# Performance work log

Measured on AMD Instinct MI355X. Metric: run time of the kernel, lower is better.

The kernel has to match this reference:

```python
import jax, jax.numpy as jnp
import numpy as np

N = 1000      # num_nodes (<= max_nodes=1000 so the dense matrix path runs)
D = 128       # input_dim
H = 128       # hidden_dim
K = 10        # num_clusters
E = 500000    # num_edges
TEMP = 1.0
EPS = 1e-5    # torch LayerNorm default eps


def setup_inputs() -> dict:
    key = jax.random.key(0)
    ks = jax.random.split(key, 10)
    w = lambda k, shape: jax.random.normal(k, shape, jnp.float32) * 0.05
    return {
        "x": jax.random.normal(ks[0], (N, D), jnp.float32),
        "edge_index": jax.random.randint(ks[1], (2, E), 0, N, dtype=jnp.int32),
        # cluster_net: Linear(D,H) LN ReLU Linear(H,H//2) LN ReLU Linear(H//2,K)
        "w1": w(ks[2], (D, H)), "b1": jnp.zeros((H,), jnp.float32),
        "g1": jnp.ones((H,), jnp.float32), "be1": jnp.zeros((H,), jnp.float32),
        "w2": w(ks[3], (H, H // 2)), "b2": jnp.zeros((H // 2,), jnp.float32),
        "g2": jnp.ones((H // 2,), jnp.float32), "be2": jnp.zeros((H // 2,), jnp.float32),
        "w3": w(ks[4], (H // 2, K)), "b3": jnp.zeros((K,), jnp.float32),
        # complementarity_net: Linear(2D,H) LN ReLU Linear(H,1) Tanh
        "cw1": w(ks[5], (2 * D, H)), "cb1": jnp.zeros((H,), jnp.float32),
        "cg1": jnp.ones((H,), jnp.float32), "cbe1": jnp.zeros((H,), jnp.float32),
        "cw2": w(ks[6], (H, 1)), "cb2": jnp.zeros((1,), jnp.float32),
        "prototypes": jax.random.normal(ks[7], (K, D), jnp.float32),
    }


def _ln(x, g, b):
    m = x.mean(-1, keepdims=True)
    v = ((x - m) ** 2).mean(-1, keepdims=True)
    return (x - m) * jax.lax.rsqrt(v + EPS) * g + b


def _forward(x, w1, b1, g1, be1, w2, b2, g2, be2, w3, b3,
             cw1, cb1, cg1, cbe1, cw2, cb2, prototypes, edge_index):
    # --- cluster_net (dropout inactive in eval) ---
    h = jax.nn.relu(_ln(x @ w1 + b1, g1, be1))
    h = jax.nn.relu(_ln(h @ w2 + b2, g2, be2))
    cluster_logits = h @ w3 + b3                       # [N, K]
    cluster_probs = jax.nn.softmax(cluster_logits / TEMP, axis=-1)

    # --- complementarity scores on edges: gather + MLP ---
    row, col = edge_index[0], edge_index[1]
    ef = jnp.concatenate([x[row], x[col]], axis=-1)    # [E, 2D]
    he = jax.nn.relu(_ln(ef @ cw1 + cb1, cg1, cbe1))   # [E, H]
    comp_scores = jnp.tanh(he @ cw2 + cb2)[:, 0]       # [E]

    # --- cluster centers from soft assignments ---
    weighted_sum = cluster_probs.T @ x                 # [K, D]
    weights_sum = cluster_probs.sum(0)[:, None] + 1e-8
    cluster_centers = weighted_sum / weights_sum

    # --- dense all-pairs complementarity matrix (N <= 1000) ---
    # concat([x_i, x_j]) @ cw1 == x_i @ cw1[:D] + x_j @ cw1[D:]
    hi = x @ cw1[:D]                                   # [N, H]
    hj = x @ cw1[D:]                                   # [N, H]
    hp = hi[:, None, :] + hj[None, :, :] + cb1         # [N, N, H]
    hp = jax.nn.relu(_ln(hp, cg1, cbe1))
    comp_matrix = jnp.tanh(hp @ cw2 + cb2)[..., 0]     # [N, N]

    return cluster_logits, cluster_probs, comp_scores, comp_matrix, cluster_centers, prototypes


def reference(x, edge_index, w1, b1, g1, be1, w2, b2, g2, be2, w3, b3,
              cw1, cb1, cg1, cbe1, cw2, cb2, prototypes):
    return _forward(x, w1, b1, g1, be1, w2, b2, g2, be2, w3, b3,
                    cw1, cb1, cg1, cbe1, cw2, cb2, prototypes, edge_index)
```

## Files before the change

kernel.cpp:

```cpp
#include <hip/hip_runtime.h>
#include <hip/hip_bf16.h>
#include <math.h>

#define NN 1000
#define DD 128
#define HH 128
#define H2 64
#define KK 10
#define EE 500000
#define LN_EPS 1e-5f

typedef float v2f __attribute__((ext_vector_type(2)));

#define OFF_LOGITS  0
#define OFF_PROBS   10000
#define OFF_SCORES  20000
#define OFF_MATRIX  520000
#define OFF_CENTERS 1520000
#define OFF_PROTO   1521280

__device__ __forceinline__ unsigned int pack_bf16x2(float a, float b) {
  unsigned int ua = __float_as_uint(a);
  unsigned int ub = __float_as_uint(b);
  ua = (ua + 0x7FFFu + ((ua >> 16) & 1u)) >> 16;
  ub = (ub + 0x7FFFu + ((ub >> 16) & 1u)) & 0xFFFF0000u;
  return ua | ub;
}

__device__ __forceinline__ v2f unpk(unsigned int u) {
  v2f r;
  r.x = __uint_as_float(u << 16);
  r.y = __uint_as_float(u & 0xFFFF0000u);
  return r;
}

__global__ __launch_bounds__(256) void k1_split(
    const float* __restrict__ x,
    const float* __restrict__ w1, const float* __restrict__ b1,
    const float* __restrict__ g1, const float* __restrict__ be1,
    const float* __restrict__ w2, const float* __restrict__ b2,
    const float* __restrict__ g2, const float* __restrict__ be2,
    const float* __restrict__ w3, const float* __restrict__ b3,
    const float* __restrict__ cw1, const float* __restrict__ cb1,
    float* __restrict__ out_logits, float* __restrict__ out_probs,
    float* __restrict__ hi, float* __restrict__ hjbT,
    float* __restrict__ Srow, float* __restrict__ Qrow,
    float* __restrict__ Tcol, float* __restrict__ Rcol) {
  const int b = blockIdx.x;
  const int t = threadIdx.x;

  if (b < NN) {
    __shared__ float sx[DD];
    __shared__ float red[8];
    if (t < 32) *(float4*)&sx[4 * t] = *(const float4*)&x[b * DD + 4 * t];
    __syncthreads();

    float a0 = 0.f, a1 = 0.f, a2 = 0.f, a3 = 0.f;
    const float* wcol = (t < 128) ? (cw1 + t) : (cw1 + DD * HH + (t - 128));
#pragma unroll 8
    for (int d = 0; d < DD; d += 4) {
      const float4 xv = *(const float4*)&sx[d];
      a0 = fmaf(xv.x, wcol[(d + 0) * HH], a0);
      a1 = fmaf(xv.y, wcol[(d + 1) * HH], a1);
      a2 = fmaf(xv.z, wcol[(d + 2) * HH], a2);
      a3 = fmaf(xv.w, wcol[(d + 3) * HH], a3);
    }
    float acc = (a0 + a1) + (a2 + a3);
    if (t >= 128) acc += cb1[t - 128];
    if (t < 128) hi[b * HH + t] = acc;
    else         hjbT[(t - 128) * NN + b] = acc;

    float s = acc, q = acc * acc;
#pragma unroll
    for (int o = 1; o < 64; o <<= 1) {
      s += __shfl_xor(s, o, 64);
      q += __shfl_xor(q, o, 64);
    }
    const int wid = t >> 6;
    if ((t & 63) == 0) { red[wid * 2] = s; red[wid * 2 + 1] = q; }
    __syncthreads();
    if (t == 0)   { Srow[b] = red[0] + red[2]; Qrow[b] = red[1] + red[3]; }
    if (t == 128) { Tcol[b] = red[4] + red[6]; Rcol[b] = red[5] + red[7]; }
  } else {
    __shared__ float sx2[2][DD];
    __shared__ float shh[2][HH];
    __shared__ float sh2[2][H2];
    __shared__ float redc[8];
    __shared__ float slg2[2][16];
    const int m = b - NN;
    const int r0 = 2 * m;
    if (t < 32)      *(float4*)&sx2[0][4 * t] = *(const float4*)&x[r0 * DD + 4 * t];
    else if (t < 64) *(float4*)&sx2[1][4 * (t - 32)] =
                         *(const float4*)&x[(r0 + 1) * DD + 4 * (t - 32)];
    __syncthreads();

    const int row = t >> 7;
    const int col = t & 127;

    float a0 = 0.f, a1 = 0.f, a2 = 0.f, a3 = 0.f;
    const float* wc = w1 + col;
#pragma unroll 8
    for (int d = 0; d < DD; d += 4) {
      const float4 xv = *(const float4*)&sx2[row][d];
      a0 = fmaf(xv.x, wc[(d + 0) * HH], a0);
      a1 = fmaf(xv.y, wc[(d + 1) * HH], a1);
      a2 = fmaf(xv.z, wc[(d + 2) * HH], a2);
      a3 = fmaf(xv.w, wc[(d + 3) * HH], a3);
    }
    float acc = (a0 + a1) + (a2 + a3) + b1[col];
    {
      float s = acc, q = acc * acc;
#pragma unroll
      for (int o = 1; o < 64; o <<= 1) {
        s += __shfl_xor(s, o, 64);
        q += __shfl_xor(q, o, 64);
      }
      const int wid = t >> 6;
      if ((t & 63) == 0) { redc[wid * 2] = s; redc[wid * 2 + 1] = q; }
    }
    __syncthreads();
    {
      const float s = redc[4 * row] + redc[4 * row + 2];
      const float q = redc[4 * row + 1] + redc[4 * row + 3];
      const float mn = s * (1.0f / HH);
      const float var = q * (1.0f / HH) - mn * mn;
      const float rs = rsqrtf(var + LN_EPS);
      shh[row][col] = fmaxf(fmaf((acc - mn) * rs, g1[col], be1[col]), 0.0f);
    }
    __syncthreads();

    if (t < 128) {
      const int rw = t >> 6, c2 = t & 63;
      float b0 = 0.f, b1_ = 0.f, b2_ = 0.f, b3_ = 0.f;
      const float* w2c = w2 + c2;
#pragma unroll 8
      for (int d = 0; d < HH; d += 4) {
        const float4 hv = *(const float4*)&shh[rw][d];
        b0 = fmaf(hv.x, w2c[(d + 0) * H2], b0);
        b1_ = fmaf(hv.y, w2c[(d + 1) * H2], b1_);
        b2_ = fmaf(hv.z, w2c[(d + 2) * H2], b2_);
        b3_ = fmaf(hv.w, w2c[(d + 3) * H2], b3_);
      }
      float av = (b0 + b1_) + (b2_ + b3_) + b2[c2];
      float s2 = av, q2 = av * av;
#pragma unroll
      for (int o = 1; o < 64; o <<= 1) {
        s2 += __shfl_xor(s2, o, 64);
        q2 += __shfl_xor(q2, o, 64);
      }
      const float m2 = s2 * (1.0f / H2);
      const float var2 = q2 * (1.0f / H2) - m2 * m2;
      const float rs2 = rsqrtf(var2 + LN_EPS);
      sh2[rw][c2] = fmaxf(fmaf((av - m2) * rs2, g2[c2], be2[c2]), 0.0f);
    }
    __syncthreads();

    if (t < 32) {
      const int rw = t >> 4, k = t & 15;
      if (k < KK) {
        float a3_ = b3[k];
#pragma unroll
        for (int d = 0; d < H2; ++d) a3_ = fmaf(sh2[rw][d], w3[d * KK + k], a3_);
        out_logits[(r0 + rw) * KK + k] = a3_;
        slg2[rw][k] = a3_;
      }
    }
    __syncthreads();
    if (t < 32) {
      const int rw = t >> 4, k = t & 15;
      if (k < KK) {
        float mx = -1e30f;
#pragma unroll
        for (int i = 0; i < KK; ++i) mx = fmaxf(mx, slg2[rw][i]);
        float den = 0.0f;
#pragma unroll
        for (int i = 0; i < KK; ++i) den += expf(slg2[rw][i] - mx);
        out_probs[(r0 + rw) * KK + k] = expf(slg2[rw][k] - mx) / den;
      }
    }
  }
}

#define NCB 8
#define NPB 125

__global__ __launch_bounds__(128) void k_centers_part(
    const float* __restrict__ x, const float* __restrict__ probs,
    float* __restrict__ pc, float* __restrict__ pw) {
  __shared__ float sp[NCB * KK];
  const int b = blockIdx.x;
  const int t = threadIdx.x;
  const int n0 = b * NCB;
  if (t < NCB * KK) sp[t] = probs[n0 * KK + t];
  __syncthreads();
  float acc[KK];
#pragma unroll
  for (int k = 0; k < KK; ++k) acc[k] = 0.0f;
#pragma unroll
  for (int nn = 0; nn < NCB; ++nn) {
    const float xv = x[(n0 + nn) * DD + t];
#pragma unroll
    for (int k = 0; k < KK; ++k) acc[k] = fmaf(sp[nn * KK + k], xv, acc[k]);
  }
#pragma unroll
  for (int k = 0; k < KK; ++k) pc[b * (KK * DD) + k * DD + t] = acc[k];
  if (t < KK) {
    float s = 0.0f;
#pragma unroll
    for (int nn = 0; nn < NCB; ++nn) s += sp[nn * KK + t];
    pw[b * 16 + t] = s;
  }
}

#define TI 64
#define TJ 32
#define LSTRA 130
#define BSTR 130

__global__ __launch_bounds__(256) void k_matrix(
    const float* __restrict__ hi, const float* __restrict__ hjbT,
    const float* __restrict__ Srow, const float* __restrict__ Qrow,
    const float* __restrict__ Tcol, const float* __restrict__ Rcol,
    const float* __restrict__ cg1, const float* __restrict__ cbe1,
    const float* __restrict__ cw2, const float* __restrict__ cb2,
    float* __restrict__ out_mat) {
  __shared__ float sa[TI * LSTRA];
  __shared__ unsigned int sbt[16 * BSTR];
  __shared__ float sg[HH], sbe[HH], sw[HH];
  const int t = threadIdx.x;
  const int j0 = blockIdx.x * TJ;
  const int i0 = blockIdx.y * TI;

  if (t < HH) { sg[t] = cg1[t]; sbe[t] = cbe1[t]; sw[t] = cw2[t]; }
#pragma unroll
  for (int it = 0; it < TI * HH / 256; ++it) {
    const int idx = it * 256 + t;
    const int r = idx >> 7, h = idx & 127;
    int gi = i0 + r; if (gi >= NN) gi = NN - 1;
    sa[r * LSTRA + h] = hi[gi * HH + h];
  }
  {
    const int cp = t & 15;
    const int hw = t >> 4;
    const int jc = j0 + 2 * cp;
    const int c0 = (jc < NN) ? jc : NN - 1;
    const int c1 = (jc + 1 < NN) ? jc + 1 : NN - 1;
#pragma unroll
    for (int hb = 0; hb < 8; ++hb) {
      const int h = hb * 16 + hw;
      sbt[cp * BSTR + h] = pack_bf16x2(hjbT[h * NN + c0], hjbT[h * NN + c1]);
    }
  }
  __syncthreads();

  const int tr = t >> 4, tc = t & 15;
  const int ia = 4 * tr;
  const int gi0 = i0 + ia;
  const int gj0 = j0 + 2 * tc;

  float Sr[4], Qr[4];
#pragma unroll
  for (int r = 0; r < 4; ++r) {
    const int gi = (gi0 + r < NN) ? gi0 + r : NN - 1;
    Sr[r] = Srow[gi]; Qr[r] = Qrow[gi];
  }
  const int c0 = (gj0 < NN) ? gj0 : NN - 1;
  const int c1 = (gj0 + 1 < NN) ? gj0 + 1 : NN - 1;
  const v2f Tc2 = (v2f){Tcol[c0], Tcol[c1]};
  const v2f Rc2 = (v2f){Rcol[c0], Rcol[c1]};

  v2f dt[4];
#pragma unroll
  for (int r = 0; r < 4; ++r) dt[r] = (v2f){0.f, 0.f};
#pragma unroll 4
  for (int h = 0; h < HH; h += 2) {
    const uint2 bb = *(const uint2*)&sbt[tc * BSTR + h];
    const v2f bx = unpk(bb.x), by = unpk(bb.y);
#pragma unroll
    for (int r = 0; r < 4; ++r) {
      const v2f av = *(const v2f*)&sa[(ia + r) * LSTRA + h];
      dt[r] += (v2f){av.x, av.x} * bx + (v2f){av.y, av.y} * by;
    }
  }

  const float inv = 1.0f / HH;
  v2f rrv[4], nmv[4];
#pragma unroll
  for (int r = 0; r < 4; ++r) {
    const v2f mu = (Sr[r] + Tc2) * inv;
    const v2f ev2 = (Qr[r] + Rc2 + 2.0f * dt[r]) * inv;
    const v2f var = ev2 - mu * mu;
    v2f rs;
    rs.x = rsqrtf(var.x + LN_EPS);
    rs.y = rsqrtf(var.y + LN_EPS);
    rrv[r] = rs;
    nmv[r] = -mu * rs;
  }

  v2f cc[4];
#pragma unroll
  for (int r = 0; r < 4; ++r) cc[r] = (v2f){0.f, 0.f};
  const v2f vzero = (v2f){0.f, 0.f};
#pragma unroll 4
  for (int h = 0; h < HH; h += 2) {
    const uint2 bb = *(const uint2*)&sbt[tc * BSTR + h];
    const v2f bx = unpk(bb.x), by = unpk(bb.y);
    const v2f gv = *(const v2f*)&sg[h];
    const v2f bev = *(const v2f*)&sbe[h];
    const v2f wv = *(const v2f*)&sw[h];
#pragma unroll
    for (int r = 0; r < 4; ++r) {
      const v2f av = *(const v2f*)&sa[(ia + r) * LSTRA + h];
      v2f v = (v2f){av.x, av.x} + bx;
      v2f z = v * rrv[r] + nmv[r];
      z = z * (v2f){gv.x, gv.x} + (v2f){bev.x, bev.x};
      z = __builtin_elementwise_max(z, vzero);
      cc[r] += z * (v2f){wv.x, wv.x};
      v = (v2f){av.y, av.y} + by;
      z = v * rrv[r] + nmv[r];
      z = z * (v2f){gv.y, gv.y} + (v2f){bev.y, bev.y};
      z = __builtin_elementwise_max(z, vzero);
      cc[r] += z * (v2f){wv.y, wv.y};
    }
  }

  const float cb = cb2[0];
  if (gj0 < NN) {
#pragma unroll
    for (int r = 0; r < 4; ++r) {
      const int gi = gi0 + r;
      if (gi < NN) {
        float2 o;
        o.x = tanhf(cc[r].x + cb);
        o.y = tanhf(cc[r].y + cb);
        *(float2*)&out_mat[gi * NN + gj0] = o;
      }
    }
  }
}

__global__ __launch_bounds__(256) void k_tail(
    const float* __restrict__ pc, const float* __restrict__ pw,
    const float* __restrict__ proto, const int* __restrict__ ei,
    const float* __restrict__ mat,
    float* __restrict__ out_centers, float* __restrict__ out_proto,
    float* __restrict__ out_scores) {
  const int b = blockIdx.x;
  const int t = threadIdx.x;
  if (b < KK) {
    __shared__ float sred[128];
    const int k = b;
    if (t < 128) sred[t] = (t < NPB) ? pw[t * 16 + k] : 0.0f;
    __syncthreads();
    for (int o = 64; o > 0; o >>= 1) {
      if (t < o) sred[t] += sred[t + o];
      __syncthreads();
    }
    if (t < 128) {
      const float wsum = sred[0] + 1e-8f;
      float acc = 0.0f;
#pragma unroll 5
      for (int bb = 0; bb < NPB; ++bb) acc += pc[bb * (KK * DD) + k * DD + t];
      out_centers[k * DD + t] = acc / wsum;
      out_proto[k * DD + t] = proto[k * DD + t];
    }
  } else {
    const int e = (b - KK) * 256 + t;
    if (e < EE) {
      const int r = ei[e];
      const int c = ei[EE + e];
      out_scores[e] = mat[r * NN + c];
    }
  }
}

extern "C" void kernel_launch(void* const* d_in, const int* in_sizes, int n_in,
                              void* d_out, int out_size, void* d_ws, size_t ws_size,
                              hipStream_t stream) {
  const float* x    = (const float*)d_in[0];
  const int*   ei   = (const int*)d_in[1];
  const float* w1   = (const float*)d_in[2];
  const float* b1   = (const float*)d_in[3];
  const float* g1   = (const float*)d_in[4];
  const float* be1  = (const float*)d_in[5];
  const float* w2   = (const float*)d_in[6];
  const float* b2   = (const float*)d_in[7];
  const float* g2   = (const float*)d_in[8];
  const float* be2  = (const float*)d_in[9];
  const float* w3   = (const float*)d_in[10];
  const float* b3   = (const float*)d_in[11];
  const float* cw1  = (const float*)d_in[12];
  const float* cb1  = (const float*)d_in[13];
  const float* cg1  = (const float*)d_in[14];
  const float* cbe1 = (const float*)d_in[15];
  const float* cw2  = (const float*)d_in[16];
  const float* cb2  = (const float*)d_in[17];
  const float* prot = (const float*)d_in[18];

  float* out        = (float*)d_out;
  float* out_logits = out + OFF_LOGITS;
  float* out_probs  = out + OFF_PROBS;
  float* out_scores = out + OFF_SCORES;
  float* out_mat    = out + OFF_MATRIX;
  float* out_cent   = out + OFF_CENTERS;
  float* out_proto  = out + OFF_PROTO;

  float* hi   = (float*)d_ws;
  float* hjbT = hi + NN * HH;
  float* Srow = hjbT + NN * HH;
  float* Qrow = Srow + NN;
  float* Tcol = Qrow + NN;
  float* Rcol = Tcol + NN;
  float* pc   = Rcol + NN;
  float* pw   = pc + NPB * KK * DD;

  k1_split<<<NN + NN / 2, 256, 0, stream>>>(
      x, w1, b1, g1, be1, w2, b2, g2, be2, w3, b3, cw1, cb1,
      out_logits, out_probs, hi, hjbT, Srow, Qrow, Tcol, Rcol);
  k_centers_part<<<NPB, 128, 0, stream>>>(x, out_probs, pc, pw);
  dim3 g3((NN + TJ - 1) / TJ, (NN + TI - 1) / TI);
  k_matrix<<<g3, 256, 0, stream>>>(hi, hjbT, Srow, Qrow, Tcol, Rcol,
                                   cg1, cbe1, cw2, cb2, out_mat);
  k_tail<<<KK + (EE + 255) / 256, 256, 0, stream>>>(pc, pw, prot, ei, out_mat,
                                                    out_cent, out_proto, out_scores);
}
```

Before: 62.79 us.

## Store hi as bf16 and enlarge matrix tile to 64x64 with 4x4 microtile

The first kernel now writes the per-node hi projection packed as bf16 pairs, halving that buffer and its load traffic. The matrix kernel grows its j-tile from 32 to 64 columns, so each thread computes 4 rows by 4 columns. The B tile is stored h-major and the A tile as packed bf16, which gives more reuse per shared-memory load in both the dot-product and LayerNorm/ReLU passes. The LayerNorm gamma, beta and output weights are now read straight from global memory instead of shared memory. Rounding hi to bf16 adds precision error, and the larger tile launches half as many blocks and uses more registers per thread.

```diff
diff --git a/kernel.cpp b/kernel.cpp
--- a/kernel.cpp
+++ b/kernel.cpp
@@ -11,6 +11,7 @@
 #define LN_EPS 1e-5f
 
 typedef float v2f __attribute__((ext_vector_type(2)));
+typedef unsigned int uint;
 
 #define OFF_LOGITS  0
 #define OFF_PROBS   10000
@@ -19,15 +20,15 @@
 #define OFF_CENTERS 1520000
 #define OFF_PROTO   1521280
 
-__device__ __forceinline__ unsigned int pack_bf16x2(float a, float b) {
-  unsigned int ua = __float_as_uint(a);
-  unsigned int ub = __float_as_uint(b);
+__device__ __forceinline__ uint pack_bf16x2(float a, float b) {
+  uint ua = __float_as_uint(a);
+  uint ub = __float_as_uint(b);
   ua = (ua + 0x7FFFu + ((ua >> 16) & 1u)) >> 16;
   ub = (ub + 0x7FFFu + ((ub >> 16) & 1u)) & 0xFFFF0000u;
   return ua | ub;
 }
 
-__device__ __forceinline__ v2f unpk(unsigned int u) {
+__device__ __forceinline__ v2f unpk(uint u) {
   v2f r;
   r.x = __uint_as_float(u << 16);
   r.y = __uint_as_float(u & 0xFFFF0000u);
@@ -43,7 +44,7 @@
     const float* __restrict__ w3, const float* __restrict__ b3,
     const float* __restrict__ cw1, const float* __restrict__ cb1,
     float* __restrict__ out_logits, float* __restrict__ out_probs,
-    float* __restrict__ hi, float* __restrict__ hjbT,
+    uint* __restrict__ hi_bf, float* __restrict__ hjbT,
     float* __restrict__ Srow, float* __restrict__ Qrow,
     float* __restrict__ Tcol, float* __restrict__ Rcol) {
   const int b = blockIdx.x;
@@ -67,8 +68,12 @@
     }
     float acc = (a0 + a1) + (a2 + a3);
     if (t >= 128) acc += cb1[t - 128];
-    if (t < 128) hi[b * HH + t] = acc;
-    else         hjbT[(t - 128) * NN + b] = acc;
+    if (t < 128) {
+      const float other = __shfl_xor(acc, 1, 64);
+      if ((t & 1) == 0) hi_bf[b * 64 + (t >> 1)] = pack_bf16x2(acc, other);
+    } else {
+      hjbT[(t - 128) * NN + b] = acc;
+    }
 
     float s = acc, q = acc * acc;
 #pragma unroll
@@ -213,42 +218,40 @@
 }
 
 #define TI 64
-#define TJ 32
-#define LSTRA 130
-#define BSTR 130
+#define TJ 64
+#define SA_STR 66
+#define SB_STR 34
 
 __global__ __launch_bounds__(256) void k_matrix(
-    const float* __restrict__ hi, const float* __restrict__ hjbT,
+    const uint* __restrict__ hi_bf, const float* __restrict__ hjbT,
     const float* __restrict__ Srow, const float* __restrict__ Qrow,
     const float* __restrict__ Tcol, const float* __restrict__ Rcol,
     const float* __restrict__ cg1, const float* __restrict__ cbe1,
     const float* __restrict__ cw2, const float* __restrict__ cb2,
     float* __restrict__ out_mat) {
-  __shared__ float sa[TI * LSTRA];
-  __shared__ unsigned int sbt[16 * BSTR];
-  __shared__ float sg[HH], sbe[HH], sw[HH];
+  __shared__ uint sa[TI * SA_STR];
+  __shared__ uint sbt[HH * SB_STR];
   const int t = threadIdx.x;
   const int j0 = blockIdx.x * TJ;
   const int i0 = blockIdx.y * TI;
 
-  if (t < HH) { sg[t] = cg1[t]; sbe[t] = cbe1[t]; sw[t] = cw2[t]; }
-#pragma unroll
-  for (int it = 0; it < TI * HH / 256; ++it) {
+#pragma unroll
+  for (int it = 0; it < 8; ++it) {
     const int idx = it * 256 + t;
-    const int r = idx >> 7, h = idx & 127;
+    const int r = idx >> 5, w2 = idx & 31;
     int gi = i0 + r; if (gi >= NN) gi = NN - 1;
-    sa[r * LSTRA + h] = hi[gi * HH + h];
+    *(uint2*)&sa[r * SA_STR + 2 * w2] = *(const uint2*)&hi_bf[gi * 64 + 2 * w2];
   }
   {
-    const int cp = t & 15;
-    const int hw = t >> 4;
+    const int cp = t & 31;
+    const int hw = t >> 5;
     const int jc = j0 + 2 * cp;
     const int c0 = (jc < NN) ? jc : NN - 1;
     const int c1 = (jc + 1 < NN) ? jc + 1 : NN - 1;
 #pragma unroll
-    for (int hb = 0; hb < 8; ++hb) {
-      const int h = hb * 16 + hw;
-      sbt[cp * BSTR + h] = pack_bf16x2(hjbT[h * NN + c0], hjbT[h * NN + c1]);
+    for (int hb = 0; hb < 16; ++hb) {
+      const int h = hb * 8 + hw;
+      sbt[h * SB_STR + cp] = pack_bf16x2(hjbT[h * NN + c0], hjbT[h * NN + c1]);
     }
   }
   __syncthreads();
@@ -256,7 +259,7 @@
   const int tr = t >> 4, tc = t & 15;
   const int ia = 4 * tr;
   const int gi0 = i0 + ia;
-  const int gj0 = j0 + 2 * tc;
+  const int gj0 = j0 + 4 * tc;
 
   float Sr[4], Qr[4];
 #pragma unroll
@@ -264,63 +267,93 @@
     const int gi = (gi0 + r < NN) ? gi0 + r : NN - 1;
     Sr[r] = Srow[gi]; Qr[r] = Qrow[gi];
   }
-  const int c0 = (gj0 < NN) ? gj0 : NN - 1;
-  const int c1 = (gj0 + 1 < NN) ? gj0 + 1 : NN - 1;
-  const v2f Tc2 = (v2f){Tcol[c0], Tcol[c1]};
-  const v2f Rc2 = (v2f){Rcol[c0], Rcol[c1]};
-
-  v2f dt[4];
-#pragma unroll
-  for (int r = 0; r < 4; ++r) dt[r] = (v2f){0.f, 0.f};
-#pragma unroll 4
-  for (int h = 0; h < HH; h += 2) {
-    const uint2 bb = *(const uint2*)&sbt[tc * BSTR + h];
-    const v2f bx = unpk(bb.x), by = unpk(bb.y);
+  v2f Tc2[2], Rc2[2];
+#pragma unroll
+  for (int p = 0; p < 2; ++p) {
+    const int ca = (gj0 + 2 * p < NN) ? gj0 + 2 * p : NN - 1;
+    const int cbx = (gj0 + 2 * p + 1 < NN) ? gj0 + 2 * p + 1 : NN - 1;
+    Tc2[p] = (v2f){Tcol[ca], Tcol[cbx]};
+    Rc2[p] = (v2f){Rcol[ca], Rcol[cbx]};
+  }
+
+  v2f dt[4][2];
+#pragma unroll
+  for (int r = 0; r < 4; ++r) { dt[r][0] = (v2f){0, 0}; dt[r][1] = (v2f){0, 0}; }
+
+#pragma unroll 2
+  for (int h = 0; h < HH; h += 4) {
+    float ar[4][4];
 #pragma unroll
     for (int r = 0; r < 4; ++r) {
-      const v2f av = *(const v2f*)&sa[(ia + r) * LSTRA + h];
-      dt[r] += (v2f){av.x, av.x} * bx + (v2f){av.y, av.y} * by;
+      const uint2 au = *(const uint2*)&sa[(ia + r) * SA_STR + (h >> 1)];
+      const v2f a01 = unpk(au.x), a23 = unpk(au.y);
+      ar[r][0] = a01.x; ar[r][1] = a01.y; ar[r][2] = a23.x; ar[r][3] = a23.y;
+    }
+#pragma unroll
+    for (int hh = 0; hh < 4; ++hh) {
+      const uint2 bu = *(const uint2*)&sbt[(h + hh) * SB_STR + 2 * tc];
+      const v2f b0 = unpk(bu.x), b1 = unpk(bu.y);
+#pragma unroll
+      for (int r = 0; r < 4; ++r) {
+        const v2f as = (v2f){ar[r][hh], ar[r][hh]};
+        dt[r][0] += as * b0;
+        dt[r][1] += as * b1;
+      }
     }
   }
 
   const float inv = 1.0f / HH;
-  v2f rrv[4], nmv[4];
-#pragma unroll
-  for (int r = 0; r < 4; ++r) {
-    const v2f mu = (Sr[r] + Tc2) * inv;
-    const v2f ev2 = (Qr[r] + Rc2 + 2.0f * dt[r]) * inv;
-    const v2f var = ev2 - mu * mu;
-    v2f rs;
-    rs.x = rsqrtf(var.x + LN_EPS);
-    rs.y = rsqrtf(var.y + LN_EPS);
-    rrv[r] = rs;
-    nmv[r] = -mu * rs;
-  }
-
-  v2f cc[4];
-#pragma unroll
-  for (int r = 0; r < 4; ++r) cc[r] = (v2f){0.f, 0.f};
+  v2f rrv[4][2], nmv[4][2];
+#pragma unroll
+  for (int r = 0; r < 4; ++r)
+#pragma unroll
+    for (int p = 0; p < 2; ++p) {
+      const v2f mu = (Sr[r] + Tc2[p]) * inv;
+      const v2f ev2 = (Qr[r] + Rc2[p] + 2.0f * dt[r][p]) * inv;
+      const v2f var = ev2 - mu * mu;
+      v2f rs;
+      rs.x = rsqrtf(var.x + LN_EPS);
+      rs.y = rsqrtf(var.y + LN_EPS);
+      rrv[r][p] = rs;
+      nmv[r][p] = -mu * rs;
+    }
+
+  v2f cc[4][2];
+#pragma unroll
+  for (int r = 0; r < 4; ++r) { cc[r][0] = (v2f){0, 0}; cc[r][1] = (v2f){0, 0}; }
   const v2f vzero = (v2f){0.f, 0.f};
-#pragma unroll 4
-  for (int h = 0; h < HH; h += 2) {
-    const uint2 bb = *(const uint2*)&sbt[tc * BSTR + h];
-    const v2f bx = unpk(bb.x), by = unpk(bb.y);
-    const v2f gv = *(const v2f*)&sg[h];
-    const v2f bev = *(const v2f*)&sbe[h];
-    const v2f wv = *(const v2f*)&sw[h];
+
+#pragma unroll 2
+  for (int h = 0; h < HH; h += 4) {
+    float ar[4][4];
 #pragma unroll
     for (int r = 0; r < 4; ++r) {
-      const v2f av = *(const v2f*)&sa[(ia + r) * LSTRA + h];
-      v2f v = (v2f){av.x, av.x} + bx;
-      v2f z = v * rrv[r] + nmv[r];
-      z = z * (v2f){gv.x, gv.x} + (v2f){bev.x, bev.x};
-      z = __builtin_elementwise_max(z, vzero);
-      cc[r] += z * (v2f){wv.x, wv.x};
-      v = (v2f){av.y, av.y} + by;
-      z = v * rrv[r] + nmv[r];
-      z = z * (v2f){gv.y, gv.y} + (v2f){bev.y, bev.y};
-      z = __builtin_elementwise_max(z, vzero);
-      cc[r] += z * (v2f){wv.y, wv.y};
+      const uint2 au = *(const uint2*)&sa[(ia + r) * SA_STR + (h >> 1)];
+      const v2f a01 = unpk(au.x), a23 = unpk(au.y);
+      ar[r][0] = a01.x; ar[r][1] = a01.y; ar[r][2] = a23.x; ar[r][3] = a23.y;
+    }
+#pragma unroll
+    for (int hh = 0; hh < 4; ++hh) {
+      const uint2 bu = *(const uint2*)&sbt[(h + hh) * SB_STR + 2 * tc];
+      const v2f b0 = unpk(bu.x), b1 = unpk(bu.y);
+      const float g_ = cg1[h + hh];
+      const float be_ = cbe1[h + hh];
+      const float w_ = cw2[h + hh];
+      const v2f gs = (v2f){g_, g_};
+      const v2f bes = (v2f){be_, be_};
+      const v2f wss = (v2f){w_, w_};
+#pragma unroll
+      for (int r = 0; r < 4; ++r) {
+        const v2f as = (v2f){ar[r][hh], ar[r][hh]};
+        v2f z0 = (as + b0) * rrv[r][0] + nmv[r][0];
+        z0 = z0 * gs + bes;
+        z0 = __builtin_elementwise_max(z0, vzero);
+        cc[r][0] += z0 * wss;
+        v2f z1 = (as + b1) * rrv[r][1] + nmv[r][1];
+        z1 = z1 * gs + bes;
+        z1 = __builtin_elementwise_max(z1, vzero);
+        cc[r][1] += z1 * wss;
+      }
     }
   }
 
@@ -330,10 +363,12 @@
     for (int r = 0; r < 4; ++r) {
       const int gi = gi0 + r;
       if (gi < NN) {
-        float2 o;
-        o.x = tanhf(cc[r].x + cb);
-        o.y = tanhf(cc[r].y + cb);
-        *(float2*)&out_mat[gi * NN + gj0] = o;
+        float4 o;
+        o.x = tanhf(cc[r][0].x + cb);
+        o.y = tanhf(cc[r][0].y + cb);
+        o.z = tanhf(cc[r][1].x + cb);
+        o.w = tanhf(cc[r][1].y + cb);
+        *(float4*)&out_mat[gi * NN + gj0] = o;
       }
     }
   }
@@ -405,21 +440,21 @@
   float* out_cent   = out + OFF_CENTERS;
   float* out_proto  = out + OFF_PROTO;
 
-  float* hi   = (float*)d_ws;
-  float* hjbT = hi + NN * HH;
-  float* Srow = hjbT + NN * HH;
-  float* Qrow = Srow + NN;
-  float* Tcol = Qrow + NN;
-  float* Rcol = Tcol + NN;
-  float* pc   = Rcol + NN;
-  float* pw   = pc + NPB * KK * DD;
+  uint*  hi_bf = (uint*)d_ws;
+  float* hjbT  = (float*)d_ws + NN * 64;
+  float* Srow  = hjbT + NN * HH;
+  float* Qrow  = Srow + NN;
+  float* Tcol  = Qrow + NN;
+  float* Rcol  = Tcol + NN;
+  float* pc    = Rcol + NN;
+  float* pw    = pc + NPB * KK * DD;
 
   k1_split<<<NN + NN / 2, 256, 0, stream>>>(
       x, w1, b1, g1, be1, w2, b2, g2, be2, w3, b3, cw1, cb1,
-      out_logits, out_probs, hi, hjbT, Srow, Qrow, Tcol, Rcol);
+      out_logits, out_probs, hi_bf, hjbT, Srow, Qrow, Tcol, Rcol);
   k_centers_part<<<NPB, 128, 0, stream>>>(x, out_probs, pc, pw);
   dim3 g3((NN + TJ - 1) / TJ, (NN + TI - 1) / TI);
-  k_matrix<<<g3, 256, 0, stream>>>(hi, hjbT, Srow, Qrow, Tcol, Rcol,
+  k_matrix<<<g3, 256, 0, stream>>>(hi_bf, hjbT, Srow, Qrow, Tcol, Rcol,
                                    cg1, cbe1, cw2, cb2, out_mat);
   k_tail<<<KK + (EE + 255) / 256, 256, 0, stream>>>(pc, pw, prot, ei, out_mat,
                                                     out_cent, out_proto, out_scores);
```

New measurement: 67.10 us. 6.9% more time.

## Retile pairwise matrix kernel to 32x64 with fp32 column operand in LDS

Applied to the files above, without the earlier changes.

The pairwise complementarity kernel switches from a 64x32 tile with bf16-packed column features to a 32x64 tile that stores the column features as fp32 in LDS with an h-major layout. Each thread now computes 2 rows by 4 columns, reading float4 column vectors and writing float4 outputs. LN gamma, beta and weight now come from global/scalar loads instead of LDS. This drops the bf16 pack/unpack overhead and the precision loss, at the cost of a larger LDS footprint (about 51KB), which may reduce occupancy.

```diff
diff --git a/kernel.cpp b/kernel.cpp
--- a/kernel.cpp
+++ b/kernel.cpp
@@ -18,21 +18,6 @@
 #define OFF_MATRIX  520000
 #define OFF_CENTERS 1520000
 #define OFF_PROTO   1521280
-
-__device__ __forceinline__ unsigned int pack_bf16x2(float a, float b) {
-  unsigned int ua = __float_as_uint(a);
-  unsigned int ub = __float_as_uint(b);
-  ua = (ua + 0x7FFFu + ((ua >> 16) & 1u)) >> 16;
-  ub = (ub + 0x7FFFu + ((ub >> 16) & 1u)) & 0xFFFF0000u;
-  return ua | ub;
-}
-
-__device__ __forceinline__ v2f unpk(unsigned int u) {
-  v2f r;
-  r.x = __uint_as_float(u << 16);
-  r.y = __uint_as_float(u & 0xFFFF0000u);
-  return r;
-}
 
 __global__ __launch_bounds__(256) void k1_split(
     const float* __restrict__ x,
@@ -212,10 +197,10 @@
   }
 }
 
-#define TI 64
-#define TJ 32
-#define LSTRA 130
-#define BSTR 130
+#define TI 32
+#define TJ 64
+#define SA_STR 130
+#define SB_STR 68
 
 __global__ __launch_bounds__(256) void k_matrix(
     const float* __restrict__ hi, const float* __restrict__ hjbT,
@@ -224,116 +209,135 @@
     const float* __restrict__ cg1, const float* __restrict__ cbe1,
     const float* __restrict__ cw2, const float* __restrict__ cb2,
     float* __restrict__ out_mat) {
-  __shared__ float sa[TI * LSTRA];
-  __shared__ unsigned int sbt[16 * BSTR];
-  __shared__ float sg[HH], sbe[HH], sw[HH];
+  __shared__ float sa[TI * SA_STR];
+  __shared__ float sb[HH * SB_STR];
   const int t = threadIdx.x;
   const int j0 = blockIdx.x * TJ;
   const int i0 = blockIdx.y * TI;
 
-  if (t < HH) { sg[t] = cg1[t]; sbe[t] = cbe1[t]; sw[t] = cw2[t]; }
-#pragma unroll
-  for (int it = 0; it < TI * HH / 256; ++it) {
+#pragma unroll
+  for (int it = 0; it < 4; ++it) {
     const int idx = it * 256 + t;
-    const int r = idx >> 7, h = idx & 127;
+    const int r = idx >> 5, w = idx & 31;
     int gi = i0 + r; if (gi >= NN) gi = NN - 1;
-    sa[r * LSTRA + h] = hi[gi * HH + h];
+    *(float4*)&sa[r * SA_STR + 4 * w] = *(const float4*)&hi[gi * HH + 4 * w];
   }
   {
-    const int cp = t & 15;
-    const int hw = t >> 4;
-    const int jc = j0 + 2 * cp;
-    const int c0 = (jc < NN) ? jc : NN - 1;
-    const int c1 = (jc + 1 < NN) ? jc + 1 : NN - 1;
-#pragma unroll
-    for (int hb = 0; hb < 8; ++hb) {
-      const int h = hb * 16 + hw;
-      sbt[cp * BSTR + h] = pack_bf16x2(hjbT[h * NN + c0], hjbT[h * NN + c1]);
+    const int c = t & 63;
+    const int hw = t >> 6;
+    int gj = j0 + c; if (gj >= NN) gj = NN - 1;
+#pragma unroll
+    for (int hb = 0; hb < 32; ++hb) {
+      const int h = hb * 4 + hw;
+      sb[h * SB_STR + c] = hjbT[h * NN + gj];
     }
   }
   __syncthreads();
 
   const int tr = t >> 4, tc = t & 15;
-  const int ia = 4 * tr;
+  const int ia = 2 * tr;
+  const int ja = 4 * tc;
   const int gi0 = i0 + ia;
-  const int gj0 = j0 + 2 * tc;
-
-  float Sr[4], Qr[4];
-#pragma unroll
-  for (int r = 0; r < 4; ++r) {
+  const int gj0 = j0 + ja;
+
+  float Sr[2], Qr[2];
+#pragma unroll
+  for (int r = 0; r < 2; ++r) {
     const int gi = (gi0 + r < NN) ? gi0 + r : NN - 1;
     Sr[r] = Srow[gi]; Qr[r] = Qrow[gi];
   }
-  const int c0 = (gj0 < NN) ? gj0 : NN - 1;
-  const int c1 = (gj0 + 1 < NN) ? gj0 + 1 : NN - 1;
-  const v2f Tc2 = (v2f){Tcol[c0], Tcol[c1]};
-  const v2f Rc2 = (v2f){Rcol[c0], Rcol[c1]};
-
-  v2f dt[4];
-#pragma unroll
-  for (int r = 0; r < 4; ++r) dt[r] = (v2f){0.f, 0.f};
+  v2f Tc2[2], Rc2[2];
+#pragma unroll
+  for (int p = 0; p < 2; ++p) {
+    const int ca = (gj0 + 2 * p < NN) ? gj0 + 2 * p : NN - 1;
+    const int cb_ = (gj0 + 2 * p + 1 < NN) ? gj0 + 2 * p + 1 : NN - 1;
+    Tc2[p] = (v2f){Tcol[ca], Tcol[cb_]};
+    Rc2[p] = (v2f){Rcol[ca], Rcol[cb_]};
+  }
+
+  v2f dt[2][2];
+#pragma unroll
+  for (int r = 0; r < 2; ++r) { dt[r][0] = (v2f){0, 0}; dt[r][1] = (v2f){0, 0}; }
+
 #pragma unroll 4
   for (int h = 0; h < HH; h += 2) {
-    const uint2 bb = *(const uint2*)&sbt[tc * BSTR + h];
-    const v2f bx = unpk(bb.x), by = unpk(bb.y);
-#pragma unroll
-    for (int r = 0; r < 4; ++r) {
-      const v2f av = *(const v2f*)&sa[(ia + r) * LSTRA + h];
-      dt[r] += (v2f){av.x, av.x} * bx + (v2f){av.y, av.y} * by;
-    }
+    const v2f a0 = *(const v2f*)&sa[(ia + 0) * SA_STR + h];
+    const v2f a1 = *(const v2f*)&sa[(ia + 1) * SA_STR + h];
+    const float4 blo = *(const float4*)&sb[h * SB_STR + ja];
+    const float4 bhi = *(const float4*)&sb[(h + 1) * SB_STR + ja];
+    const v2f b0l = (v2f){blo.x, blo.y}, b1l = (v2f){blo.z, blo.w};
+    const v2f b0h = (v2f){bhi.x, bhi.y}, b1h = (v2f){bhi.z, bhi.w};
+    dt[0][0] += (v2f){a0.x, a0.x} * b0l + (v2f){a0.y, a0.y} * b0h;
+    dt[0][1] += (v2f){a0.x, a0.x} * b1l + (v2f){a0.y, a0.y} * b1h;
+    dt[1][0] += (v2f){a1.x, a1.x} * b0l + (v2f){a1.y, a1.y} * b0h;
+    dt[1][1] += (v2f){a1.x, a1.x} * b1l + (v2f){a1.y, a1.y} * b1h;
   }
 
   const float inv = 1.0f / HH;
-  v2f rrv[4], nmv[4];
-#pragma unroll
-  for (int r = 0; r < 4; ++r) {
-    const v2f mu = (Sr[r] + Tc2) * inv;
-    const v2f ev2 = (Qr[r] + Rc2 + 2.0f * dt[r]) * inv;
-    const v2f var = ev2 - mu * mu;
-    v2f rs;
-    rs.x = rsqrtf(var.x + LN_EPS);
-    rs.y = rsqrtf(var.y + LN_EPS);
-    rrv[r] = rs;
-    nmv[r] = -mu * rs;
-  }
-
-  v2f cc[4];
-#pragma unroll
-  for (int r = 0; r < 4; ++r) cc[r] = (v2f){0.f, 0.f};
+  v2f rrv[2][2], nmv[2][2];
+#pragma unroll
+  for (int r = 0; r < 2; ++r)
+#pragma unroll
+    for (int p = 0; p < 2; ++p) {
+      const v2f mu = (Sr[r] + Tc2[p]) * inv;
+      const v2f ev2 = (Qr[r] + Rc2[p] + 2.0f * dt[r][p]) * inv;
+      const v2f var = ev2 - mu * mu;
+      v2f rs;
+      rs.x = rsqrtf(var.x + LN_EPS);
+      rs.y = rsqrtf(var.y + LN_EPS);
+      rrv[r][p] = rs;
+      nmv[r][p] = -mu * rs;
+    }
+
+  v2f cc[2][2];
+#pragma unroll
+  for (int r = 0; r < 2; ++r) { cc[r][0] = (v2f){0, 0}; cc[r][1] = (v2f){0, 0}; }
   const v2f vzero = (v2f){0.f, 0.f};
+
 #pragma unroll 4
   for (int h = 0; h < HH; h += 2) {
-    const uint2 bb = *(const uint2*)&sbt[tc * BSTR + h];
-    const v2f bx = unpk(bb.x), by = unpk(bb.y);
-    const v2f gv = *(const v2f*)&sg[h];
-    const v2f bev = *(const v2f*)&sbe[h];
-    const v2f wv = *(const v2f*)&sw[h];
-#pragma unroll
-    for (int r = 0; r < 4; ++r) {
-      const v2f av = *(const v2f*)&sa[(ia + r) * LSTRA + h];
-      v2f v = (v2f){av.x, av.x} + bx;
-      v2f z = v * rrv[r] + nmv[r];
-      z = z * (v2f){gv.x, gv.x} + (v2f){bev.x, bev.x};
-      z = __builtin_elementwise_max(z, vzero);
-      cc[r] += z * (v2f){wv.x, wv.x};
-      v = (v2f){av.y, av.y} + by;
-      z = v * rrv[r] + nmv[r];
-      z = z * (v2f){gv.y, gv.y} + (v2f){bev.y, bev.y};
-      z = __builtin_elementwise_max(z, vzero);
-      cc[r] += z * (v2f){wv.y, wv.y};
+    const v2f a0 = *(const v2f*)&sa[(ia + 0) * SA_STR + h];
+    const v2f a1 = *(const v2f*)&sa[(ia + 1) * SA_STR + h];
+    const float4 blo = *(const float4*)&sb[h * SB_STR + ja];
+    const float4 bhi = *(const float4*)&sb[(h + 1) * SB_STR + ja];
+    const float g0 = cg1[h], g1_ = cg1[h + 1];
+    const float e0 = cbe1[h], e1 = cbe1[h + 1];
+    const float w0 = cw2[h], w1_ = cw2[h + 1];
+    const v2f b0l = (v2f){blo.x, blo.y}, b1l = (v2f){blo.z, blo.w};
+    const v2f b0h = (v2f){bhi.x, bhi.y}, b1h = (v2f){bhi.z, bhi.w};
+#pragma unroll
+    for (int r = 0; r < 2; ++r) {
+      const v2f ar = (r == 0) ? a0 : a1;
+      const v2f axl = (v2f){ar.x, ar.x};
+      const v2f axh = (v2f){ar.y, ar.y};
+#pragma unroll
+      for (int p = 0; p < 2; ++p) {
+        const v2f bl = (p == 0) ? b0l : b1l;
+        const v2f bh = (p == 0) ? b0h : b1h;
+        v2f z = (axl + bl) * rrv[r][p] + nmv[r][p];
+        z = z * (v2f){g0, g0} + (v2f){e0, e0};
+        z = __builtin_elementwise_max(z, vzero);
+        cc[r][p] += z * (v2f){w0, w0};
+        z = (axh + bh) * rrv[r][p] + nmv[r][p];
+        z = z * (v2f){g1_, g1_} + (v2f){e1, e1};
+        z = __builtin_elementwise_max(z, vzero);
+        cc[r][p] += z * (v2f){w1_, w1_};
+      }
     }
   }
 
   const float cb = cb2[0];
   if (gj0 < NN) {
 #pragma unroll
-    for (int r = 0; r < 4; ++r) {
+    for (int r = 0; r < 2; ++r) {
       const int gi = gi0 + r;
       if (gi < NN) {
-        float2 o;
-        o.x = tanhf(cc[r].x + cb);
-        o.y = tanhf(cc[r].y + cb);
-        *(float2*)&out_mat[gi * NN + gj0] = o;
+        float4 o;
+        o.x = tanhf(cc[r][0].x + cb);
+        o.y = tanhf(cc[r][0].y + cb);
+        o.z = tanhf(cc[r][1].x + cb);
+        o.w = tanhf(cc[r][1].y + cb);
+        *(float4*)&out_mat[gi * NN + gj0] = o;
       }
     }
   }
```

New measurement: 60.65 us. 3.4% less time.

## Store hi tile as bf16 in LDS, batch two rows per projection block

Applied to the files above, without the earlier changes.

The matrix kernel now packs the row-side hidden projections into bf16 pairs in shared memory, halving LDS footprint and traffic. Its inner loops read 128-bit chunks and process four hidden units per iteration. The LayerNorm gamma/beta and output weights are read straight from global memory instead of being staged in LDS. The projection kernel computes two nodes per block, so it reuses each loaded weight twice and launches half as many blocks. These changes trade the precision of hi (now bf16) for less LDS bandwidth and occupancy pressure.

```diff
diff --git a/kernel.cpp b/kernel.cpp
--- a/kernel.cpp
+++ b/kernel.cpp
@@ -11,6 +11,7 @@
 #define LN_EPS 1e-5f
 
 typedef float v2f __attribute__((ext_vector_type(2)));
+typedef unsigned int uint;
 
 #define OFF_LOGITS  0
 #define OFF_PROBS   10000
@@ -19,15 +20,15 @@
 #define OFF_CENTERS 1520000
 #define OFF_PROTO   1521280
 
-__device__ __forceinline__ unsigned int pack_bf16x2(float a, float b) {
-  unsigned int ua = __float_as_uint(a);
-  unsigned int ub = __float_as_uint(b);
+__device__ __forceinline__ uint pack_bf16x2(float a, float b) {
+  uint ua = __float_as_uint(a);
+  uint ub = __float_as_uint(b);
   ua = (ua + 0x7FFFu + ((ua >> 16) & 1u)) >> 16;
   ub = (ub + 0x7FFFu + ((ub >> 16) & 1u)) & 0xFFFF0000u;
   return ua | ub;
 }
 
-__device__ __forceinline__ v2f unpk(unsigned int u) {
+__device__ __forceinline__ v2f unpk(uint u) {
   v2f r;
   r.x = __uint_as_float(u << 16);
   r.y = __uint_as_float(u & 0xFFFF0000u);
@@ -49,45 +50,63 @@
   const int b = blockIdx.x;
   const int t = threadIdx.x;
 
-  if (b < NN) {
-    __shared__ float sx[DD];
-    __shared__ float red[8];
-    if (t < 32) *(float4*)&sx[4 * t] = *(const float4*)&x[b * DD + 4 * t];
-    __syncthreads();
-
-    float a0 = 0.f, a1 = 0.f, a2 = 0.f, a3 = 0.f;
-    const float* wcol = (t < 128) ? (cw1 + t) : (cw1 + DD * HH + (t - 128));
+  if (b < NN / 2) {
+    __shared__ float sx2[2][DD];
+    __shared__ float red[16];
+    const int r0 = 2 * b;
+    if (t < 64) {
+      const int rr = t >> 5, c4 = t & 31;
+      *(float4*)&sx2[rr][4 * c4] = *(const float4*)&x[(r0 + rr) * DD + 4 * c4];
+    }
+    __syncthreads();
+
+    const int col = t & 127;
+    const float* wcol = (t < 128) ? (cw1 + col) : (cw1 + DD * HH + col);
+    float p00 = 0.f, p01 = 0.f, p10 = 0.f, p11 = 0.f;
 #pragma unroll 8
-    for (int d = 0; d < DD; d += 4) {
-      const float4 xv = *(const float4*)&sx[d];
-      a0 = fmaf(xv.x, wcol[(d + 0) * HH], a0);
-      a1 = fmaf(xv.y, wcol[(d + 1) * HH], a1);
-      a2 = fmaf(xv.z, wcol[(d + 2) * HH], a2);
-      a3 = fmaf(xv.w, wcol[(d + 3) * HH], a3);
-    }
-    float acc = (a0 + a1) + (a2 + a3);
-    if (t >= 128) acc += cb1[t - 128];
-    if (t < 128) hi[b * HH + t] = acc;
-    else         hjbT[(t - 128) * NN + b] = acc;
-
-    float s = acc, q = acc * acc;
+    for (int d = 0; d < DD; d += 2) {
+      const float w0 = wcol[d * HH];
+      const float w1_ = wcol[(d + 1) * HH];
+      const float2 x0 = *(const float2*)&sx2[0][d];
+      const float2 x1 = *(const float2*)&sx2[1][d];
+      p00 = fmaf(x0.x, w0, p00); p01 = fmaf(x0.y, w1_, p01);
+      p10 = fmaf(x1.x, w0, p10); p11 = fmaf(x1.y, w1_, p11);
+    }
+    float acc0 = p00 + p01, acc1 = p10 + p11;
+    if (t >= 128) { const float cb_ = cb1[col]; acc0 += cb_; acc1 += cb_; }
+    if (t < 128) {
+      hi[(r0 + 0) * HH + col] = acc0;
+      hi[(r0 + 1) * HH + col] = acc1;
+    } else {
+      *(float2*)&hjbT[col * NN + r0] = (float2){acc0, acc1};
+    }
+    float s0 = acc0, q0 = acc0 * acc0, s1 = acc1, q1 = acc1 * acc1;
 #pragma unroll
     for (int o = 1; o < 64; o <<= 1) {
-      s += __shfl_xor(s, o, 64);
-      q += __shfl_xor(q, o, 64);
+      s0 += __shfl_xor(s0, o, 64); q0 += __shfl_xor(q0, o, 64);
+      s1 += __shfl_xor(s1, o, 64); q1 += __shfl_xor(q1, o, 64);
     }
     const int wid = t >> 6;
-    if ((t & 63) == 0) { red[wid * 2] = s; red[wid * 2 + 1] = q; }
-    __syncthreads();
-    if (t == 0)   { Srow[b] = red[0] + red[2]; Qrow[b] = red[1] + red[3]; }
-    if (t == 128) { Tcol[b] = red[4] + red[6]; Rcol[b] = red[5] + red[7]; }
+    if ((t & 63) == 0) {
+      red[wid * 4 + 0] = s0; red[wid * 4 + 1] = q0;
+      red[wid * 4 + 2] = s1; red[wid * 4 + 3] = q1;
+    }
+    __syncthreads();
+    if (t == 0) {
+      Srow[r0] = red[0] + red[4];  Qrow[r0] = red[1] + red[5];
+      Srow[r0 + 1] = red[2] + red[6]; Qrow[r0 + 1] = red[3] + red[7];
+    }
+    if (t == 128) {
+      Tcol[r0] = red[8] + red[12];  Rcol[r0] = red[9] + red[13];
+      Tcol[r0 + 1] = red[10] + red[14]; Rcol[r0 + 1] = red[11] + red[15];
+    }
   } else {
     __shared__ float sx2[2][DD];
     __shared__ float shh[2][HH];
     __shared__ float sh2[2][H2];
     __shared__ float redc[8];
     __shared__ float slg2[2][16];
-    const int m = b - NN;
+    const int m = b - NN / 2;
     const int r0 = 2 * m;
     if (t < 32)      *(float4*)&sx2[0][4 * t] = *(const float4*)&x[r0 * DD + 4 * t];
     else if (t < 64) *(float4*)&sx2[1][4 * (t - 32)] =
@@ -214,8 +233,8 @@
 
 #define TI 64
 #define TJ 32
-#define LSTRA 130
-#define BSTR 130
+#define SA_STR 66
+#define SB_STR 132
 
 __global__ __launch_bounds__(256) void k_matrix(
     const float* __restrict__ hi, const float* __restrict__ hjbT,
@@ -224,20 +243,19 @@
     const float* __restrict__ cg1, const float* __restrict__ cbe1,
     const float* __restrict__ cw2, const float* __restrict__ cb2,
     float* __restrict__ out_mat) {
-  __shared__ float sa[TI * LSTRA];
-  __shared__ unsigned int sbt[16 * BSTR];
-  __shared__ float sg[HH], sbe[HH], sw[HH];
+  __shared__ uint sa[TI * SA_STR];
+  __shared__ uint sb[16 * SB_STR];
   const int t = threadIdx.x;
   const int j0 = blockIdx.x * TJ;
   const int i0 = blockIdx.y * TI;
 
-  if (t < HH) { sg[t] = cg1[t]; sbe[t] = cbe1[t]; sw[t] = cw2[t]; }
-#pragma unroll
-  for (int it = 0; it < TI * HH / 256; ++it) {
+#pragma unroll
+  for (int it = 0; it < 16; ++it) {
     const int idx = it * 256 + t;
-    const int r = idx >> 7, h = idx & 127;
+    const int r = idx >> 6, w = idx & 63;
     int gi = i0 + r; if (gi >= NN) gi = NN - 1;
-    sa[r * LSTRA + h] = hi[gi * HH + h];
+    const float2 av = *(const float2*)&hi[gi * HH + 2 * w];
+    sa[r * SA_STR + w] = pack_bf16x2(av.x, av.y);
   }
   {
     const int cp = t & 15;
@@ -248,7 +266,7 @@
 #pragma unroll
     for (int hb = 0; hb < 8; ++hb) {
       const int h = hb * 16 + hw;
-      sbt[cp * BSTR + h] = pack_bf16x2(hjbT[h * NN + c0], hjbT[h * NN + c1]);
+      sb[cp * SB_STR + h] = pack_bf16x2(hjbT[h * NN + c0], hjbT[h * NN + c1]);
     }
   }
   __syncthreads();
@@ -264,22 +282,25 @@
     const int gi = (gi0 + r < NN) ? gi0 + r : NN - 1;
     Sr[r] = Srow[gi]; Qr[r] = Qrow[gi];
   }
-  const int c0 = (gj0 < NN) ? gj0 : NN - 1;
-  const int c1 = (gj0 + 1 < NN) ? gj0 + 1 : NN - 1;
-  const v2f Tc2 = (v2f){Tcol[c0], Tcol[c1]};
-  const v2f Rc2 = (v2f){Rcol[c0], Rcol[c1]};
+  const int cc0 = (gj0 < NN) ? gj0 : NN - 1;
+  const int cc1 = (gj0 + 1 < NN) ? gj0 + 1 : NN - 1;
+  const v2f Tc2 = (v2f){Tcol[cc0], Tcol[cc1]};
+  const v2f Rc2 = (v2f){Rcol[cc0], Rcol[cc1]};
 
   v2f dt[4];
 #pragma unroll
   for (int r = 0; r < 4; ++r) dt[r] = (v2f){0.f, 0.f};
-#pragma unroll 4
-  for (int h = 0; h < HH; h += 2) {
-    const uint2 bb = *(const uint2*)&sbt[tc * BSTR + h];
-    const v2f bx = unpk(bb.x), by = unpk(bb.y);
+
+#pragma unroll 2
+  for (int h = 0; h < HH; h += 4) {
+    const uint4 bu = *(const uint4*)&sb[tc * SB_STR + h];
+    const v2f b0 = unpk(bu.x), b1 = unpk(bu.y), b2_ = unpk(bu.z), b3_ = unpk(bu.w);
 #pragma unroll
     for (int r = 0; r < 4; ++r) {
-      const v2f av = *(const v2f*)&sa[(ia + r) * LSTRA + h];
-      dt[r] += (v2f){av.x, av.x} * bx + (v2f){av.y, av.y} * by;
+      const uint2 au = *(const uint2*)&sa[(ia + r) * SA_STR + (h >> 1)];
+      const v2f a01 = unpk(au.x), a23 = unpk(au.y);
+      dt[r] += (v2f){a01.x, a01.x} * b0 + (v2f){a01.y, a01.y} * b1
+             + (v2f){a23.x, a23.x} * b2_ + (v2f){a23.y, a23.y} * b3_;
     }
   }
 
@@ -301,26 +322,35 @@
 #pragma unroll
   for (int r = 0; r < 4; ++r) cc[r] = (v2f){0.f, 0.f};
   const v2f vzero = (v2f){0.f, 0.f};
-#pragma unroll 4
-  for (int h = 0; h < HH; h += 2) {
-    const uint2 bb = *(const uint2*)&sbt[tc * BSTR + h];
-    const v2f bx = unpk(bb.x), by = unpk(bb.y);
-    const v2f gv = *(const v2f*)&sg[h];
-    const v2f bev = *(const v2f*)&sbe[h];
-    const v2f wv = *(const v2f*)&sw[h];
+
+#pragma unroll 2
+  for (int h = 0; h < HH; h += 4) {
+    const uint4 bu = *(const uint4*)&sb[tc * SB_STR + h];
+    const v2f b0 = unpk(bu.x), b1 = unpk(bu.y), b2_ = unpk(bu.z), b3_ = unpk(bu.w);
+    const float4 gq = *(const float4*)&cg1[h];
+    const float4 eq = *(const float4*)&cbe1[h];
+    const float4 wq = *(const float4*)&cw2[h];
 #pragma unroll
     for (int r = 0; r < 4; ++r) {
-      const v2f av = *(const v2f*)&sa[(ia + r) * LSTRA + h];
-      v2f v = (v2f){av.x, av.x} + bx;
-      v2f z = v * rrv[r] + nmv[r];
-      z = z * (v2f){gv.x, gv.x} + (v2f){bev.x, bev.x};
+      const uint2 au = *(const uint2*)&sa[(ia + r) * SA_STR + (h >> 1)];
+      const v2f a01 = unpk(au.x), a23 = unpk(au.y);
+      v2f z;
+      z = ((v2f){a01.x, a01.x} + b0) * rrv[r] + nmv[r];
+      z = z * (v2f){gq.x, gq.x} + (v2f){eq.x, eq.x};
       z = __builtin_elementwise_max(z, vzero);
-      cc[r] += z * (v2f){wv.x, wv.x};
-      v = (v2f){av.y, av.y} + by;
-      z = v * rrv[r] + nmv[r];
-      z = z * (v2f){gv.y, gv.y} + (v2f){bev.y, bev.y};
+      cc[r] += z * (v2f){wq.x, wq.x};
+      z = ((v2f){a01.y, a01.y} + b1) * rrv[r] + nmv[r];
+      z = z * (v2f){gq.y, gq.y} + (v2f){eq.y, eq.y};
       z = __builtin_elementwise_max(z, vzero);
-      cc[r] += z * (v2f){wv.y, wv.y};
+      cc[r] += z * (v2f){wq.y, wq.y};
+      z = ((v2f){a23.x, a23.x} + b2_) * rrv[r] + nmv[r];
+      z = z * (v2f){gq.z, gq.z} + (v2f){eq.z, eq.z};
+      z = __builtin_elementwise_max(z, vzero);
+      cc[r] += z * (v2f){wq.z, wq.z};
+      z = ((v2f){a23.y, a23.y} + b3_) * rrv[r] + nmv[r];
+      z = z * (v2f){gq.w, gq.w} + (v2f){eq.w, eq.w};
+      z = __builtin_elementwise_max(z, vzero);
+      cc[r] += z * (v2f){wq.w, wq.w};
     }
   }
 
@@ -414,7 +444,7 @@
   float* pc   = Rcol + NN;
   float* pw   = pc + NPB * KK * DD;
 
-  k1_split<<<NN + NN / 2, 256, 0, stream>>>(
+  k1_split<<<NN, 256, 0, stream>>>(
       x, w1, b1, g1, be1, w2, b2, g2, be2, w3, b3, cw1, cb1,
       out_logits, out_probs, hi, hjbT, Srow, Qrow, Tcol, Rcol);
   k_centers_part<<<NPB, 128, 0, stream>>>(x, out_probs, pc, pw);
```

Result: no change. 62.88 us (+0.1%).
